# Kernel optimization log

Measured on AMD Instinct MI355X. Metric: run time of the kernel, lower is better.

Reference implementation:

```python
import jax, jax.numpy as jnp
import numpy as np

M, N, K = 1024, 11008, 4096


def _unpack_i2u(Bp):
    """Unpack 2-bit unsigned weights per decode_i2u_to_i8s interleave.

    Bp: [N, K//4] int8 storage. Within each group of 4 bytes (16 elements),
    output element at position 4*i + j = (byte_j >> (2*i)) & 3.
    Returns [N, K] int8 with values in {0,1,2,3}.
    """
    Bu = jax.lax.bitcast_convert_type(Bp, jnp.uint8)  # [N, K//4]
    n, kc = Bu.shape
    Bg = Bu.reshape(n, kc // 4, 1, 4)                 # [N, G, 1, j]
    shifts = (jnp.arange(4, dtype=jnp.uint8) * jnp.uint8(2)).reshape(1, 1, 4, 1)
    vals = (Bg >> shifts) & jnp.uint8(3)              # [N, G, i, j]
    return vals.reshape(n, kc * 4).astype(jnp.int8)   # [N, K]


def setup_inputs() -> dict:
    key = jax.random.key(0)
    k1, k2 = jax.random.split(key)
    A = jax.random.randint(k1, (M, K), -128, 128, dtype=jnp.int8)
    B = jax.random.randint(k2, (N, K // 4), -128, 128, dtype=jnp.int8)
    return {"A": A, "B": B}


def reference(A, B):
    W = _unpack_i2u(B)  # [N, K] int8
    C = jax.lax.dot_general(
        A, W,
        dimension_numbers=(((1,), (1,)), ((), ())),
        preferred_element_type=jnp.int32,
    )  # [M, N] int32
    return C
```

## Files before the change

kernel.cpp:

```cpp
#include <hip/hip_runtime.h>
#include <stdint.h>


#define MM 1024
#define NN 11008
#define KK 4096
#define KSTEPS 64
#define MTILES (MM / 128)
#define NTILES (NN / 128)
#define NWAVES (16 * NTILES)

using i32x4  = __attribute__((ext_vector_type(4))) int;
using i32x16 = __attribute__((ext_vector_type(16))) int;

__device__ __forceinline__ int pack4(i32x4 v) {
    return (int)(((uint32_t)v[0] & 0xFFu) | (((uint32_t)v[1] & 0xFFu) << 8)
               | (((uint32_t)v[2] & 0xFFu) << 16) | (((uint32_t)v[3] & 0xFFu) << 24));
}

__global__ __launch_bounds__(256) void prep_A(const int* __restrict__ src,
                                              uint8_t* __restrict__ dst) {
    const int g = blockIdx.x * 256 + threadIdx.x;
    const int kstep = g >> 12;
    const int rem   = g & 4095;
    const int mtile = rem >> 9;
    const int c     = rem & 511;
    const int row32 = (c >> 7) & 3, kk2 = (c >> 6) & 1;
    const int lane  = c & 63;
    const int row   = mtile * 128 + row32 * 32 + (lane & 31);
    const int kbyte = kstep * 64 + kk2 * 32 + (lane >> 5) * 16;
    const i32x4* s4 = (const i32x4*)(src + (size_t)row * KK + kbyte);
    i32x4 o;
#pragma unroll
    for (int q = 0; q < 4; ++q) o[q] = pack4(s4[q]);
    *(i32x4*)(dst + (size_t)g * 16) = o;
}

__global__ __launch_bounds__(256) void prep_B(const int* __restrict__ src,
                                              uint8_t* __restrict__ dst) {
    const int t = blockIdx.x * 256 + threadIdx.x;
    const int lane = t & 63;
    const int wc   = (t >> 6) & 1;
    const int rem  = t >> 7;
    const int ntile = rem % NTILES;
    const int kstep = rem / NTILES;
    const int l31 = lane & 31, h = lane >> 5;
    i32x4 o;
#pragma unroll
    for (int q = 0; q < 4; ++q) {
        const int ni = q >> 1, kk2 = q & 1;
        const int n  = ntile * 128 + wc * 64 + ni * 32 + l31;
        const i32x4 v = *(const i32x4*)(src + (size_t)n * (KK / 4) + kstep * 16 + kk2 * 8 + h * 4);
        o[q] = pack4(v);
    }
    *(i32x4*)(dst + (size_t)t * 16) = o;
}

struct Bfrag { i32x4 c0, c1; };

__global__ __launch_bounds__(64, 2) void bitnet_gemm(const uint8_t* __restrict__ A2,
                                                     const uint8_t* __restrict__ B3,
                                                     int* __restrict__ C) {
    const int lane = threadIdx.x;
    const int l31  = lane & 31, h = lane >> 5;

    const int bid = blockIdx.x;
    const int l   = (bid & 7) * (NWAVES / 8) + (bid >> 3);
    const int wm  = l & 15;
    const int wn  = l >> 4;
    const int mtile = wm >> 1, half = wm & 1;

    const size_t strideA = (size_t)MTILES * 8192;
    const size_t strideB = (size_t)NTILES * 2048;

    const uint8_t* pa[4];
#pragma unroll
    for (int s = 0; s < 4; ++s) {
        const int mi = s >> 1, kk2 = s & 1;
        pa[s] = A2 + (size_t)mtile * 8192 + ((half * 2 + mi) * 2 + kk2) * 1024 + lane * 16;
    }
    const uint8_t* pb = B3 + (size_t)wn * 2048 + lane * 16;

    i32x16 acc[2][4] = {};
    i32x4 fa0[4], fa1[4];
    Bfrag fp0, fp1;

    auto LOAD = [&](i32x4 (&a)[4], Bfrag& p, int ks) {
#pragma unroll
        for (int s = 0; s < 4; ++s)
            a[s] = *(const i32x4*)(pa[s] + (size_t)ks * strideA);
        p.c0 = *(const i32x4*)(pb + (size_t)ks * strideB);
        p.c1 = *(const i32x4*)(pb + (size_t)ks * strideB + 1024);
    };

    auto COMPUTE = [&](const i32x4 (&a)[4], const Bfrag& p) {
#pragma unroll
        for (int kk2 = 0; kk2 < 2; ++kk2) {
#pragma unroll
            for (int nc = 0; nc < 4; ++nc) {
                const uint32_t q = (uint32_t)((nc < 2 ? p.c0 : p.c1)[(nc & 1) * 2 + kk2]);
                i32x4 b;
#pragma unroll
                for (int i = 0; i < 4; ++i)
                    b[i] = (int)((q >> (2 * i)) & 0x03030303u);
                acc[0][nc] = __builtin_amdgcn_mfma_i32_32x32x32_i8(a[0 + kk2], b, acc[0][nc], 0, 0, 0);
                acc[1][nc] = __builtin_amdgcn_mfma_i32_32x32x32_i8(a[2 + kk2], b, acc[1][nc], 0, 0, 0);
            }
        }
    };

    LOAD(fa0, fp0, 0);
    LOAD(fa1, fp1, 1);

#pragma unroll 1
    for (int ks = 0; ks < KSTEPS - 2; ks += 2) {
        COMPUTE(fa0, fp0); LOAD(fa0, fp0, ks + 2);
        COMPUTE(fa1, fp1); LOAD(fa1, fp1, ks + 3);
    }
    COMPUTE(fa0, fp0);
    COMPUTE(fa1, fp1);

    const int brow = wm * 64, bcol = wn * 128;
#pragma unroll
    for (int mi = 0; mi < 2; ++mi)
#pragma unroll
        for (int nc = 0; nc < 4; ++nc) {
            const int colg = bcol + nc * 32 + l31;
#pragma unroll
            for (int r = 0; r < 16; ++r) {
                const int rowin = (r & 3) + 8 * (r >> 2) + 4 * h;
                const int rowg  = brow + mi * 32 + rowin;
                C[(size_t)rowg * NN + colg] = acc[mi][nc][r];
            }
        }
}

extern "C" void kernel_launch(void* const* d_in, const int* in_sizes, int n_in,
                              void* d_out, int out_size, void* d_ws, size_t ws_size,
                              hipStream_t stream) {
    const int* A32 = (const int*)d_in[0];
    const int* B32 = (const int*)d_in[1];
    int* C = (int*)d_out;

    uint8_t* A2 = (uint8_t*)d_ws;
    uint8_t* B3 = A2 + (size_t)MM * KK;

    prep_A<<<dim3((MM * KK / 16) / 256), dim3(256), 0, stream>>>(A32, A2);
    prep_B<<<dim3((NN * 64) / 256), dim3(256), 0, stream>>>(B32, B3);
    bitnet_gemm<<<dim3(NWAVES), dim3(64), 0, stream>>>(A2, B3, C);
}
```

Baseline: 69.84 us.

## Split K across two waves per block with LDS reduction; coalesce prep_B reads

```diff
diff --git a/kernel.cpp b/kernel.cpp
--- a/kernel.cpp
+++ b/kernel.cpp
@@ -8,7 +8,7 @@
 #define KSTEPS 64
 #define MTILES (MM / 128)
 #define NTILES (NN / 128)
-#define NWAVES (16 * NTILES)
+#define NBLOCKS (16 * NTILES)
 
 using i32x4  = __attribute__((ext_vector_type(4))) int;
 using i32x16 = __attribute__((ext_vector_type(16))) int;
@@ -39,47 +39,44 @@
 __global__ __launch_bounds__(256) void prep_B(const int* __restrict__ src,
                                               uint8_t* __restrict__ dst) {
     const int t = blockIdx.x * 256 + threadIdx.x;
-    const int lane = t & 63;
-    const int wc   = (t >> 6) & 1;
-    const int rem  = t >> 7;
-    const int ntile = rem % NTILES;
-    const int kstep = rem / NTILES;
-    const int l31 = lane & 31, h = lane >> 5;
-    i32x4 o;
+    const int n = t >> 6, kstep = t & 63;
+    const int ntile = n >> 7, wc = (n >> 6) & 1, ni = (n >> 5) & 1, l31 = n & 31;
+    const i32x4* s4 = (const i32x4*)(src + (size_t)n * (KK / 4) + kstep * 16);
+    int w[4];
 #pragma unroll
-    for (int q = 0; q < 4; ++q) {
-        const int ni = q >> 1, kk2 = q & 1;
-        const int n  = ntile * 128 + wc * 64 + ni * 32 + l31;
-        const i32x4 v = *(const i32x4*)(src + (size_t)n * (KK / 4) + kstep * 16 + kk2 * 8 + h * 4);
-        o[q] = pack4(v);
-    }
-    *(i32x4*)(dst + (size_t)t * 16) = o;
+    for (int j = 0; j < 4; ++j) w[j] = pack4(s4[j]);
+    uint8_t* base = dst + ((size_t)kstep * NTILES + ntile) * 2048 + wc * 1024;
+    *(int2*)(base + l31 * 16 + ni * 8)        = make_int2(w[0], w[2]);
+    *(int2*)(base + (l31 + 32) * 16 + ni * 8) = make_int2(w[1], w[3]);
 }
 
 struct Bfrag { i32x4 c0, c1; };
 
-__global__ __launch_bounds__(64, 2) void bitnet_gemm(const uint8_t* __restrict__ A2,
-                                                     const uint8_t* __restrict__ B3,
-                                                     int* __restrict__ C) {
-    const int lane = threadIdx.x;
+__global__ __launch_bounds__(128, 2) void bitnet_gemm(const uint8_t* __restrict__ A2,
+                                                      const uint8_t* __restrict__ B3,
+                                                      int* __restrict__ C) {
+    const int tid  = threadIdx.x;
+    const int lane = tid & 63, wid = tid >> 6;
     const int l31  = lane & 31, h = lane >> 5;
 
     const int bid = blockIdx.x;
-    const int l   = (bid & 7) * (NWAVES / 8) + (bid >> 3);
+    const int l   = (bid & 7) * (NBLOCKS / 8) + (bid >> 3);
     const int wm  = l & 15;
     const int wn  = l >> 4;
     const int mtile = wm >> 1, half = wm & 1;
 
     const size_t strideA = (size_t)MTILES * 8192;
     const size_t strideB = (size_t)NTILES * 2048;
+    const int ksbase = wid * (KSTEPS / 2);
 
     const uint8_t* pa[4];
 #pragma unroll
     for (int s = 0; s < 4; ++s) {
         const int mi = s >> 1, kk2 = s & 1;
-        pa[s] = A2 + (size_t)mtile * 8192 + ((half * 2 + mi) * 2 + kk2) * 1024 + lane * 16;
+        pa[s] = A2 + (size_t)ksbase * strideA + (size_t)mtile * 8192
+              + ((half * 2 + mi) * 2 + kk2) * 1024 + lane * 16;
     }
-    const uint8_t* pb = B3 + (size_t)wn * 2048 + lane * 16;
+    const uint8_t* pb = B3 + (size_t)ksbase * strideB + (size_t)wn * 2048 + lane * 16;
 
     i32x16 acc[2][4] = {};
     i32x4 fa0[4], fa1[4];
@@ -113,26 +110,52 @@
     LOAD(fa1, fp1, 1);
 
 #pragma unroll 1
-    for (int ks = 0; ks < KSTEPS - 2; ks += 2) {
+    for (int ks = 0; ks < KSTEPS / 2 - 2; ks += 2) {
         COMPUTE(fa0, fp0); LOAD(fa0, fp0, ks + 2);
         COMPUTE(fa1, fp1); LOAD(fa1, fp1, ks + 3);
     }
     COMPUTE(fa0, fp0);
     COMPUTE(fa1, fp1);
 
-    const int brow = wm * 64, bcol = wn * 128;
+    __shared__ __align__(16) i32x4 red[8 * 4 * 64];
+    if (wid == 1) {
 #pragma unroll
-    for (int mi = 0; mi < 2; ++mi)
+        for (int mi = 0; mi < 2; ++mi)
 #pragma unroll
-        for (int nc = 0; nc < 4; ++nc) {
-            const int colg = bcol + nc * 32 + l31;
+            for (int nc = 0; nc < 4; ++nc) {
+                const i32x16 v = acc[mi][nc];
 #pragma unroll
-            for (int r = 0; r < 16; ++r) {
-                const int rowin = (r & 3) + 8 * (r >> 2) + 4 * h;
-                const int rowg  = brow + mi * 32 + rowin;
-                C[(size_t)rowg * NN + colg] = acc[mi][nc][r];
+                for (int q = 0; q < 4; ++q) {
+                    i32x4 s;
+                    s[0] = v[q * 4 + 0]; s[1] = v[q * 4 + 1];
+                    s[2] = v[q * 4 + 2]; s[3] = v[q * 4 + 3];
+                    red[((mi * 4 + nc) * 4 + q) * 64 + lane] = s;
+                }
             }
-        }
+    }
+    __syncthreads();
+    if (wid == 0) {
+        const int brow = wm * 64, bcol = wn * 128;
+#pragma unroll
+        for (int mi = 0; mi < 2; ++mi)
+#pragma unroll
+            for (int nc = 0; nc < 4; ++nc) {
+                i32x16 v = acc[mi][nc];
+#pragma unroll
+                for (int q = 0; q < 4; ++q) {
+                    const i32x4 r = red[((mi * 4 + nc) * 4 + q) * 64 + lane];
+                    v[q * 4 + 0] += r[0]; v[q * 4 + 1] += r[1];
+                    v[q * 4 + 2] += r[2]; v[q * 4 + 3] += r[3];
+                }
+                const int colg = bcol + nc * 32 + l31;
+#pragma unroll
+                for (int r = 0; r < 16; ++r) {
+                    const int rowin = (r & 3) + 8 * (r >> 2) + 4 * h;
+                    const int rowg  = brow + mi * 32 + rowin;
+                    C[(size_t)rowg * NN + colg] = v[r];
+                }
+            }
+    }
 }
 
 extern "C" void kernel_launch(void* const* d_in, const int* in_sizes, int n_in,
@@ -147,5 +170,5 @@
 
     prep_A<<<dim3((MM * KK / 16) / 256), dim3(256), 0, stream>>>(A32, A2);
     prep_B<<<dim3((NN * 64) / 256), dim3(256), 0, stream>>>(B32, B3);
-    bitnet_gemm<<<dim3(NWAVES), dim3(64), 0, stream>>>(A2, B3, C);
+    bitnet_gemm<<<dim3(NBLOCKS), dim3(128), 0, stream>>>(A2, B3, C);
 }
```

Result: slower. 73.51 us (+5.3%).
